# Optimization experiments

Measured on AMD Instinct MI355X. Metric: run time of the kernel, lower is better.

Reference implementation:

```python
import jax, jax.numpy as jnp
import numpy as np

N_SAMPLES = 32768
CHANNELS = 128
N_ATOMS = 512
ATOM_SIZE = 512
N_TRANSFERS = 64
TRANSFER_SIZE = 8192
N_EVENTS = 32
N_ROOMS = 8
DILATIONS = (1, 3, 9, 27, 1)
BATCH = 8


def _conv1d(x, w, padding, dil=1):
    # x: [B,C,T], w: [O,I,K]
    return jax.lax.conv_general_dilated(
        x, w, (1,), padding, rhs_dilation=(dil,),
        dimension_numbers=('NCH', 'OIH', 'NCH'))


def _fft_convolve(a, b):
    # linear convolution along last dim, truncated to original length
    n = a.shape[-1]
    af = jnp.fft.rfft(a, n=2 * n)
    bf = jnp.fft.rfft(b, n=2 * n)
    return jnp.fft.irfft(af * bf, n=2 * n)[..., :n]


def _mlp(x, hw, hb, ow, ob):
    # LinearOutputStack: 3 hidden Linear(C,C)+leaky_relu, then Linear(C,out)
    for i in range(hw.shape[0]):
        x = jax.nn.leaky_relu(x @ hw[i] + hb[i], 0.2)
    return x @ ow + ob


def setup_inputs() -> dict:
    key = jax.random.key(0)
    ks = jax.random.split(key, 25)
    s = 0.02
    C = CHANNELS
    return {
        'x': jax.random.normal(ks[0], (BATCH, 1, N_SAMPLES), jnp.float32),
        'bank': jax.random.normal(ks[1], (C, 1, 512), jnp.float32) * s,
        'w_net': jax.random.normal(ks[2], (len(DILATIONS), C, C, 3), jnp.float32) * s,
        'b_net': jnp.zeros((len(DILATIONS), C), jnp.float32),
        'attn_w': jax.random.normal(ks[3], (1, C, 1), jnp.float32) * s,
        'attn_b': jnp.zeros((1,), jnp.float32),
        'atoms_hw': jax.random.normal(ks[4], (3, C, C), jnp.float32) * s,
        'atoms_hb': jnp.zeros((3, C), jnp.float32),
        'atoms_ow': jax.random.normal(ks[5], (C, N_ATOMS), jnp.float32) * s,
        'atoms_ob': jnp.zeros((N_ATOMS,), jnp.float32),
        'trans_hw': jax.random.normal(ks[6], (3, C, C), jnp.float32) * s,
        'trans_hb': jnp.zeros((3, C), jnp.float32),
        'trans_ow': jax.random.normal(ks[7], (C, N_TRANSFERS), jnp.float32) * s,
        'trans_ob': jnp.zeros((N_TRANSFERS,), jnp.float32),
        'amp_hw': jax.random.normal(ks[8], (3, C, C), jnp.float32) * s,
        'amp_hb': jnp.zeros((3, C), jnp.float32),
        'amp_ow': jax.random.normal(ks[9], (C, 1), jnp.float32) * s,
        'amp_ob': jnp.zeros((1,), jnp.float32),
        'atoms_dict': jax.random.uniform(ks[10], (N_ATOMS, ATOM_SIZE), jnp.float32, -1.0, 1.0),
        'transfer_dict': jax.random.normal(ks[11], (N_TRANSFERS, TRANSFER_SIZE), jnp.float32) * 0.01,
        'rooms': jax.random.normal(ks[12], (N_ROOMS, N_SAMPLES), jnp.float32) * 0.01,
        'room_w': jax.random.normal(ks[13], (C, N_ROOMS), jnp.float32) * s,
        'room_b': jnp.zeros((N_ROOMS,), jnp.float32),
        'mix_w': jax.random.normal(ks[14], (C, 1), jnp.float32) * s,
        'mix_b': jnp.zeros((1,), jnp.float32),
    }


def reference(x, bank, w_net, b_net, attn_w, attn_b,
              atoms_hw, atoms_hb, atoms_ow, atoms_ob,
              trans_hw, trans_hb, trans_ow, trans_ob,
              amp_hw, amp_hb, amp_ow, amp_ob,
              atoms_dict, transfer_dict, rooms, room_w, room_b, mix_w, mix_b):
    B = x.shape[0]
    # front-end filter bank, padding=256, truncate to n_samples
    h = _conv1d(x, bank, [(256, 256)])[..., :N_SAMPLES]            # [B,C,T]
    # DilatedStack: residual dilated convs
    for i, d in enumerate(DILATIONS):
        h = h + jax.nn.leaky_relu(
            _conv1d(h, w_net[i], 'SAME', d) + b_net[i][None, :, None], 0.2)
    # ExampleNorm: per-example std normalization
    h = h / (jnp.std(h, axis=(1, 2), keepdims=True) + 1e-8)
    context = jnp.max(h, axis=-1)                                   # [B,C]
    attn = jax.nn.sigmoid(_conv1d(h, attn_w, 'SAME') + attn_b[None, :, None])[:, 0, :]  # [B,T]
    # sparsify_vectors: top-k attention positions, latents scaled by attn
    vals, idx = jax.lax.top_k(attn, N_EVENTS)                        # [B,E]
    lat = jnp.take_along_axis(jnp.swapaxes(h, 1, 2), idx[..., None], axis=1) * vals[..., None]  # [B,E,C]
    atoms = jax.nn.softmax(_mlp(lat, atoms_hw, atoms_hb, atoms_ow, atoms_ob), axis=-1) @ atoms_dict
    transfers = jax.nn.softmax(_mlp(lat, trans_hw, trans_hb, trans_ow, trans_ob), axis=-1) @ transfer_dict
    amps = _mlp(lat, amp_hw, amp_hb, amp_ow, amp_ob) ** 2            # [B,E,1]
    atoms = jnp.pad(atoms, ((0, 0), (0, 0), (0, TRANSFER_SIZE - ATOM_SIZE)))
    ev = (_fft_convolve(atoms, transfers) + atoms) * amps            # [B,E,Ts]
    # overlap-add scatter. NOTE: faithful to the original, which does
    # output[:, :, idx:idx+Ts] += x[i, e] -- every event accumulates into a
    # buffer shared across the whole batch.
    pos = idx.reshape(-1)[:, None] + jnp.arange(TRANSFER_SIZE)[None, :]  # [B*E,Ts]
    buf = jnp.zeros(2 * N_SAMPLES, ev.dtype).at[pos].add(ev.reshape(-1, TRANSFER_SIZE))
    dry = jnp.broadcast_to(buf[:N_SAMPLES][None, :], (B, N_SAMPLES))  # [B,T]
    # ReverbGenerator: context -> room choice + wet/dry mix
    impulse = jax.nn.softmax(context @ room_w + room_b, axis=-1) @ rooms  # [B,T]
    mix = jax.nn.sigmoid(context @ mix_w + mix_b)                     # [B,1]
    wet = _fft_convolve(dry, impulse)
    out = dry * (1.0 - mix) + wet * mix
    return out[:, None, :]
```

## Files before the change

### kernel.cpp

```cpp
#include <hip/hip_runtime.h>
#include <math.h>

#define TSAMP 32768
#define CCH 128
#define NBATCH 8
#define NEV 32
#define NROWS 256
#define NATOMS 512
#define ASIZE 512
#define NTRANS 64
#define TSIZE 8192

#define DRY_SCALE 16777216.0f
#define IMP_SCALE 64.0f
#define WET_DESCALE 9.313225746154785e-10f

typedef _Float16 f16x8 __attribute__((ext_vector_type(8)));
typedef _Float16 f16x4 __attribute__((ext_vector_type(4)));
typedef float f32x4 __attribute__((ext_vector_type(4)));


__global__ void k_zs(double* __restrict__ sums) {
  if (threadIdx.x < 16) sums[threadIdx.x] = 0.0;
}

__global__ __launch_bounds__(256) void k_zero(float* __restrict__ wet,
                                              float* __restrict__ dry) {
  int i = blockIdx.x * 256 + threadIdx.x;
  if (i < NBATCH * TSAMP) wet[i] = 0.f;
  if (i < TSAMP) dry[i] = 0.f;
}

__global__ __launch_bounds__(256) void k_wsplit(const float* __restrict__ wn,
                                                _Float16* __restrict__ whi,
                                                _Float16* __restrict__ wlo) {
  const int i = blockIdx.x * 256 + threadIdx.x;
  if (i >= 245760) return;
  const int ci = i & 127;
  int r = i >> 7;
  const int o = r & 127;
  r >>= 7;
  const int k = r % 3;
  const int l = r / 3;
  const float w = wn[(((size_t)l*128 + o)*128 + ci)*3 + k];
  const _Float16 hi = (_Float16)w;
  whi[i] = hi;
  wlo[i] = (_Float16)(w - (float)hi);
}

__global__ __launch_bounds__(256) void k_bsplit(const float* __restrict__ bank,
                                                _Float16* __restrict__ bhi,
                                                _Float16* __restrict__ blo) {
  const int i = blockIdx.x * 256 + threadIdx.x;
  if (i < 65536) {
    const float w = bank[i];
    const _Float16 hi = (_Float16)w;
    bhi[i] = hi;
    blo[i] = (_Float16)(w - (float)hi);
  }
}

__global__ __launch_bounds__(256) void k_front_mfma(
    const float* __restrict__ x, const _Float16* __restrict__ bhi,
    const _Float16* __restrict__ blo, float* __restrict__ h) {
  __shared__ _Float16 shi[8*664];
  __shared__ _Float16 slo[8*664];
  const int t0 = blockIdx.x * 128;
  const int b  = blockIdx.y;
  const float* xb = x + (size_t)b*TSAMP;
  const int tid = threadIdx.x;

  for (int flat = tid; flat < 8*632; flat += 256) {
    const int p = flat / 632;
    const int q = flat - p*632;
    const int g = t0 - 256 + q + p;
    const float v = (g >= 0 && g < TSAMP) ? xb[g] : 0.f;
    const _Float16 hi = (_Float16)v;
    shi[p*664 + q] = hi;
    slo[p*664 + q] = (_Float16)(v - (float)hi);
  }
  __syncthreads();

  const int wv = tid >> 6;
  const int lane = tid & 63;
  const int n = lane & 15;
  const int quad = lane >> 4;
  const int c0 = wv * 32;
  const int ph = n & 7;
  const int nb = n & 8;

  f32x4 acc[2][8];
#pragma unroll
  for (int i = 0; i < 2; ++i)
#pragma unroll
    for (int j = 0; j < 8; ++j) acc[i][j] = (f32x4){0.f,0.f,0.f,0.f};

  for (int kc = 0; kc < 16; ++kc) {
    const int kb = kc*32 + quad*8;
    f16x8 ahi[2], alo[2];
#pragma unroll
    for (int os = 0; os < 2; ++os) {
      const size_t ao = (size_t)(c0 + os*16 + n)*512 + kb;
      ahi[os] = *(const f16x8*)(bhi + ao);
      alo[os] = *(const f16x8*)(blo + ao);
    }
#pragma unroll
    for (int tg = 0; tg < 2; ++tg) {
      f16x8 xh[4], xl[4];
#pragma unroll
      for (int u = 0; u < 4; ++u) {
        const int a = ph*664 + (tg*4 + u)*16 + nb + kb;
        xh[u] = *(const f16x8*)(shi + a);
        xl[u] = *(const f16x8*)(slo + a);
      }
#pragma unroll
      for (int os = 0; os < 2; ++os)
#pragma unroll
        for (int u = 0; u < 4; ++u) {
          f32x4 a4 = acc[os][tg*4 + u];
          a4 = __builtin_amdgcn_mfma_f32_16x16x32_f16(ahi[os], xh[u], a4, 0, 0, 0);
          a4 = __builtin_amdgcn_mfma_f32_16x16x32_f16(alo[os], xh[u], a4, 0, 0, 0);
          a4 = __builtin_amdgcn_mfma_f32_16x16x32_f16(ahi[os], xl[u], a4, 0, 0, 0);
          acc[os][tg*4 + u] = a4;
        }
    }
  }

  float* hb = h + (size_t)b*TSAMP*CCH;
#pragma unroll
  for (int os = 0; os < 2; ++os) {
    const int cb = c0 + os*16 + quad*4;
#pragma unroll
    for (int ts = 0; ts < 8; ++ts) {
      const int t = t0 + ts*16 + n;
      *(f32x4*)(hb + (size_t)t*CCH + cb) = acc[os][ts];
    }
  }
}

__global__ __launch_bounds__(256) void k_dil_mfma(
    const float* __restrict__ hin0, const _Float16* __restrict__ whi,
    const _Float16* __restrict__ wlo, const float* __restrict__ bias,
    float* __restrict__ hout0, const int d) {
  extern __shared__ _Float16 sh[];
  const int twin = 64 + 2*d;
  _Float16* shi = sh;
  _Float16* slo = sh + twin*136;
  const int t0 = blockIdx.x * 64;
  const size_t bs = (size_t)blockIdx.y * CCH * TSAMP;
  const float* __restrict__ hin = hin0 + bs;
  float* __restrict__ hout = hout0 + bs;
  const int tid = threadIdx.x;

  for (int flat = tid; flat < twin*32; flat += 256) {
    const int tw = flat >> 5;
    const int c4 = (flat & 31) << 2;
    const int g = t0 - d + tw;
    float4 v = {0.f, 0.f, 0.f, 0.f};
    if (g >= 0 && g < TSAMP) v = *(const float4*)(hin + (size_t)g*CCH + c4);
    f16x4 hv, lv;
    hv[0] = (_Float16)v.x; hv[1] = (_Float16)v.y;
    hv[2] = (_Float16)v.z; hv[3] = (_Float16)v.w;
    lv[0] = (_Float16)(v.x - (float)hv[0]); lv[1] = (_Float16)(v.y - (float)hv[1]);
    lv[2] = (_Float16)(v.z - (float)hv[2]); lv[3] = (_Float16)(v.w - (float)hv[3]);
    *(f16x4*)(shi + tw*136 + c4) = hv;
    *(f16x4*)(slo + tw*136 + c4) = lv;
  }
  __syncthreads();

  const int wv = tid >> 6;
  const int lane = tid & 63;
  const int n = lane & 15;
  const int quad = lane >> 4;
  const int o0 = wv * 32;

  f32x4 acc[2][4];
#pragma unroll
  for (int i = 0; i < 2; ++i)
#pragma unroll
    for (int j = 0; j < 4; ++j) acc[i][j] = (f32x4){0.f,0.f,0.f,0.f};

  for (int k = 0; k < 3; ++k) {
    for (int kc = 0; kc < 4; ++kc) {
      const int cib = kc*32 + quad*8;
      f16x8 ahi[2], alo[2];
#pragma unroll
      for (int os = 0; os < 2; ++os) {
        const size_t wo = ((size_t)k*128 + (o0 + os*16 + n))*128 + cib;
        ahi[os] = *(const f16x8*)(whi + wo);
        alo[os] = *(const f16x8*)(wlo + wo);
      }
      f16x8 bhi[4], blo[4];
#pragma unroll
      for (int ts = 0; ts < 4; ++ts) {
        const int a = (ts*16 + n + k*d)*136 + cib;
        bhi[ts] = *(const f16x8*)(shi + a);
        blo[ts] = *(const f16x8*)(slo + a);
      }
#pragma unroll
      for (int os = 0; os < 2; ++os)
#pragma unroll
        for (int ts = 0; ts < 4; ++ts) {
          acc[os][ts] = __builtin_amdgcn_mfma_f32_16x16x32_f16(ahi[os], bhi[ts], acc[os][ts], 0, 0, 0);
          acc[os][ts] = __builtin_amdgcn_mfma_f32_16x16x32_f16(alo[os], bhi[ts], acc[os][ts], 0, 0, 0);
          acc[os][ts] = __builtin_amdgcn_mfma_f32_16x16x32_f16(ahi[os], blo[ts], acc[os][ts], 0, 0, 0);
        }
    }
  }

#pragma unroll
  for (int os = 0; os < 2; ++os) {
    const int ob = o0 + os*16 + quad*4;
    const f32x4 bs4 = *(const f32x4*)(bias + ob);
#pragma unroll
    for (int ts = 0; ts < 4; ++ts) {
      const int t = t0 + ts*16 + n;
      const int tw = ts*16 + n + d;
      const f16x4 phv = *(const f16x4*)(shi + tw*136 + ob);
      const f16x4 plv = *(const f16x4*)(slo + tw*136 + ob);
      f32x4 res;
#pragma unroll
      for (int r = 0; r < 4; ++r) {
        float v = acc[os][ts][r] + bs4[r];
        v = v > 0.f ? v : 0.2f*v;
        res[r] = (float)phv[r] + (float)plv[r] + v;
      }
      *(f32x4*)(hout + (size_t)t*CCH + ob) = res;
    }
  }
}

__global__ __launch_bounds__(256) void k_dil_last(
    const float* __restrict__ hin0, const _Float16* __restrict__ whi,
    const _Float16* __restrict__ wlo, const float* __restrict__ bias,
    float* __restrict__ hout0, const int d,
    const float* __restrict__ aw, double* __restrict__ sums,
    float* __restrict__ attnraw, float* __restrict__ pm, const int bb0) {
  extern __shared__ _Float16 sh[];
  const int twin = 64 + 2*d;
  _Float16* shi = sh;
  _Float16* slo = sh + twin*136;
  __shared__ float attl[4*64];
  __shared__ double sred[8];
  const int t0 = blockIdx.x * 64;
  const int b = bb0 + blockIdx.y;
  const size_t bs = (size_t)blockIdx.y * CCH * TSAMP;
  const float* __restrict__ hin = hin0 + bs;
  float* __restrict__ hout = hout0 + bs;
  const int tid = threadIdx.x;

  for (int flat = tid; flat < twin*32; flat += 256) {
    const int tw = flat >> 5;
    const int c4 = (flat & 31) << 2;
    const int g = t0 - d + tw;
    float4 v = {0.f, 0.f, 0.f, 0.f};
    if (g >= 0 && g < TSAMP) v = *(const float4*)(hin + (size_t)g*CCH + c4);
    f16x4 hv, lv;
    hv[0] = (_Float16)v.x; hv[1] = (_Float16)v.y;
    hv[2] = (_Float16)v.z; hv[3] = (_Float16)v.w;
    lv[0] = (_Float16)(v.x - (float)hv[0]); lv[1] = (_Float16)(v.y - (float)hv[1]);
    lv[2] = (_Float16)(v.z - (float)hv[2]); lv[3] = (_Float16)(v.w - (float)hv[3]);
    *(f16x4*)(shi + tw*136 + c4) = hv;
    *(f16x4*)(slo + tw*136 + c4) = lv;
  }
  __syncthreads();

  const int wv = tid >> 6;
  const int lane = tid & 63;
  const int n = lane & 15;
  const int quad = lane >> 4;
  const int o0 = wv * 32;

  f32x4 acc[2][4];
#pragma unroll
  for (int i = 0; i < 2; ++i)
#pragma unroll
    for (int j = 0; j < 4; ++j) acc[i][j] = (f32x4){0.f,0.f,0.f,0.f};

  for (int k = 0; k < 3; ++k) {
    for (int kc = 0; kc < 4; ++kc) {
      const int cib = kc*32 + quad*8;
      f16x8 ahi[2], alo[2];
#pragma unroll
      for (int os = 0; os < 2; ++os) {
        const size_t wo = ((size_t)k*128 + (o0 + os*16 + n))*128 + cib;
        ahi[os] = *(const f16x8*)(whi + wo);
        alo[os] = *(const f16x8*)(wlo + wo);
      }
      f16x8 bhi[4], blo[4];
#pragma unroll
      for (int ts = 0; ts < 4; ++ts) {
        const int a = (ts*16 + n + k*d)*136 + cib;
        bhi[ts] = *(const f16x8*)(shi + a);
        blo[ts] = *(const f16x8*)(slo + a);
      }
#pragma unroll
      for (int os = 0; os < 2; ++os)
#pragma unroll
        for (int ts = 0; ts < 4; ++ts) {
          acc[os][ts] = __builtin_amdgcn_mfma_f32_16x16x32_f16(ahi[os], bhi[ts], acc[os][ts], 0, 0, 0);
          acc[os][ts] = __builtin_amdgcn_mfma_f32_16x16x32_f16(alo[os], bhi[ts], acc[os][ts], 0, 0, 0);
          acc[os][ts] = __builtin_amdgcn_mfma_f32_16x16x32_f16(ahi[os], blo[ts], acc[os][ts], 0, 0, 0);
        }
    }
  }

  const f32x4 awq0 = *(const f32x4*)(aw + o0 + quad*4);
  const f32x4 awq1 = *(const f32x4*)(aw + o0 + 16 + quad*4);
  double s = 0.0, s2 = 0.0;
  float pa[4] = {0.f, 0.f, 0.f, 0.f};
  f32x4 cm[2];
  cm[0] = (f32x4){-3.4e38f, -3.4e38f, -3.4e38f, -3.4e38f};
  cm[1] = cm[0];

#pragma unroll
  for (int os = 0; os < 2; ++os) {
    const int ob = o0 + os*16 + quad*4;
    const f32x4 bs4 = *(const f32x4*)(bias + ob);
    const f32x4 awv = os ? awq1 : awq0;
#pragma unroll
    for (int ts = 0; ts < 4; ++ts) {
      const int t = t0 + ts*16 + n;
      const int tw = ts*16 + n + d;
      const f16x4 phv = *(const f16x4*)(shi + tw*136 + ob);
      const f16x4 plv = *(const f16x4*)(slo + tw*136 + ob);
      f32x4 res;
      float dotp = 0.f;
#pragma unroll
      for (int r = 0; r < 4; ++r) {
        float v = acc[os][ts][r] + bs4[r];
        v = v > 0.f ? v : 0.2f*v;
        const float hv = (float)phv[r] + (float)plv[r] + v;
        res[r] = hv;
        s += (double)hv; s2 += (double)hv*(double)hv;
        dotp += hv * awv[r];
        cm[os][r] = fmaxf(cm[os][r], hv);
      }
      pa[ts] += dotp;
      *(f32x4*)(hout + (size_t)t*CCH + ob) = res;
    }
  }

#pragma unroll
  for (int ts = 0; ts < 4; ++ts) {
    pa[ts] += __shfl_xor(pa[ts], 16);
    pa[ts] += __shfl_xor(pa[ts], 32);
  }
  if (quad == 0) {
#pragma unroll
    for (int ts = 0; ts < 4; ++ts) attl[wv*64 + ts*16 + n] = pa[ts];
  }
#pragma unroll
  for (int mk = 1; mk <= 8; mk <<= 1)
#pragma unroll
    for (int os = 0; os < 2; ++os)
#pragma unroll
      for (int r = 0; r < 4; ++r)
        cm[os][r] = fmaxf(cm[os][r], __shfl_xor(cm[os][r], mk));
  if (n == 0) {
#pragma unroll
    for (int os = 0; os < 2; ++os)
      *(f32x4*)(pm + ((size_t)b*512 + blockIdx.x)*128 + o0 + os*16 + quad*4) = cm[os];
  }
  for (int sft = 32; sft; sft >>= 1) { s += __shfl_down(s, sft); s2 += __shfl_down(s2, sft); }
  if (lane == 0) { sred[wv*2] = s; sred[wv*2+1] = s2; }
  __syncthreads();
  if (tid < 64)
    attnraw[(size_t)b*TSAMP + t0 + tid] =
        attl[tid] + attl[64 + tid] + attl[128 + tid] + attl[192 + tid];
  if (tid == 0) {
    atomicAdd(&sums[b*2],   sred[0] + sred[2] + sred[4] + sred[6]);
    atomicAdd(&sums[b*2+1], sred[1] + sred[3] + sred[5] + sred[7]);
  }
}

__global__ void k_scale(const double* __restrict__ sums, float* __restrict__ scal) {
  const int b = threadIdx.x;
  if (b < NBATCH) {
    const double n = (double)CCH * (double)TSAMP;
    const double mean = sums[b*2] / n;
    double var = sums[b*2+1] / n - mean*mean;
    if (var < 0.0) var = 0.0;
    scal[b] = (float)(1.0 / (sqrt(var) + 1e-8));
  }
}

__global__ void k_context2(const float* __restrict__ pm, const float* __restrict__ scal,
                           float* __restrict__ ctx) {
  const int b = blockIdx.x;
  const int c = threadIdx.x;
  float m = -3.4e38f;
  for (int s = 0; s < 512; ++s) m = fmaxf(m, pm[((size_t)b*512 + s)*128 + c]);
  ctx[b*128 + c] = m * scal[b];
}

__global__ __launch_bounds__(256) void k_attn2(const float* __restrict__ raw,
                                               const float* __restrict__ scal,
                                               const float* __restrict__ ab,
                                               float* __restrict__ attn) {
  const int b = blockIdx.y;
  const int i = blockIdx.x*1024 + threadIdx.x*4;
  const float s = scal[b], bb = ab[0];
  const float4 v = *(const float4*)(raw + (size_t)b*TSAMP + i);
  float* o = attn + (size_t)b*TSAMP + i;
  o[0] = 1.f/(1.f+expf(-(v.x*s+bb)));
  o[1] = 1.f/(1.f+expf(-(v.y*s+bb)));
  o[2] = 1.f/(1.f+expf(-(v.z*s+bb)));
  o[3] = 1.f/(1.f+expf(-(v.w*s+bb)));
}

__global__ __launch_bounds__(256) void k_topk1(const float* __restrict__ attn,
                                               float* __restrict__ cv,
                                               int* __restrict__ cidx) {
  const int ch = blockIdx.x, b = blockIdx.y;
  const float* a = attn + (size_t)b*TSAMP + ch*4096;
  __shared__ float v[4096];
  __shared__ float rv[4]; __shared__ int ri[4];
  const int tid = threadIdx.x;
  for (int i = tid; i < 4096; i += 256) v[i] = a[i];
  __syncthreads();
  for (int e = 0; e < NEV; ++e) {
    float bv = -1e30f; int bi = 0;
    for (int i = tid; i < 4096; i += 256) {
      const float x = v[i];
      if (x > bv) { bv = x; bi = i; }
    }
    for (int s = 32; s; s >>= 1) {
      const float ov = __shfl_down(bv, s); const int oi = __shfl_down(bi, s);
      if (ov > bv || (ov == bv && oi < bi)) { bv = ov; bi = oi; }
    }
    if ((tid & 63) == 0) { rv[tid >> 6] = bv; ri[tid >> 6] = bi; }
    __syncthreads();
    if (tid == 0) {
      int bb = 0;
      for (int w2 = 1; w2 < 4; ++w2)
        if (rv[w2] > rv[bb] || (rv[w2] == rv[bb] && ri[w2] < ri[bb])) bb = w2;
      cv[(b*8 + ch)*NEV + e] = rv[bb];
      cidx[(b*8 + ch)*NEV + e] = ch*4096 + ri[bb];
      v[ri[bb]] = -1e30f;
    }
    __syncthreads();
  }
}

__global__ __launch_bounds__(256) void k_topk2(const float* __restrict__ cv,
                                               const int* __restrict__ ci_,
                                               float* __restrict__ vals,
                                               int* __restrict__ idxs) {
  const int b = blockIdx.x;
  const int tid = threadIdx.x;
  float my = cv[b*256 + tid];
  int   mi = ci_[b*256 + tid];
  __shared__ float rv[4]; __shared__ int ri[4];
  __shared__ float bvs; __shared__ int bis;
  for (int e = 0; e < NEV; ++e) {
    float bv = my; int bi = mi;
    for (int s = 32; s; s >>= 1) {
      const float ov = __shfl_down(bv, s); const int oi = __shfl_down(bi, s);
      if (ov > bv || (ov == bv && oi < bi)) { bv = ov; bi = oi; }
    }
    if ((tid & 63) == 0) { rv[tid >> 6] = bv; ri[tid >> 6] = bi; }
    __syncthreads();
    if (tid == 0) {
      int bb = 0;
      for (int w2 = 1; w2 < 4; ++w2)
        if (rv[w2] > rv[bb] || (rv[w2] == rv[bb] && ri[w2] < ri[bb])) bb = w2;
      vals[b*NEV + e] = rv[bb]; idxs[b*NEV + e] = ri[bb];
      bvs = rv[bb]; bis = ri[bb];
    }
    __syncthreads();
    if (mi == bis && my == bvs) my = -1e30f;
    __syncthreads();
  }
}

__device__ __forceinline__ float blk_max128(float v, float* red) {
  const int tid = threadIdx.x;
  red[tid] = v; __syncthreads();
  for (int s = 64; s > 0; s >>= 1) {
    if (tid < s) red[tid] = fmaxf(red[tid], red[tid + s]);
    __syncthreads();
  }
  const float r = red[0]; __syncthreads();
  return r;
}
__device__ __forceinline__ float blk_sum128(float v, float* red) {
  const int tid = threadIdx.x;
  red[tid] = v; __syncthreads();
  for (int s = 64; s > 0; s >>= 1) {
    if (tid < s) red[tid] += red[tid + s];
    __syncthreads();
  }
  const float r = red[0]; __syncthreads();
  return r;
}
__device__ __forceinline__ float mlp_hidden3(float latv, const float* __restrict__ hw,
                                             const float* __restrict__ hb, float* xa) {
  const int tid = threadIdx.x;
  float cur = latv;
  for (int i = 0; i < 3; ++i) {
    xa[tid] = cur; __syncthreads();
    const float* W = hw + (size_t)i*CCH*CCH;
    float acc = hb[i*CCH + tid];
    for (int c = 0; c < CCH; ++c) acc += xa[c] * W[c*CCH + tid];
    cur = acc > 0.f ? acc : 0.2f*acc;
    __syncthreads();
  }
  return cur;
}

__global__ __launch_bounds__(128) void k_mlp(
    const float* __restrict__ h, const float* __restrict__ scal,
    const float* __restrict__ vals, const int* __restrict__ idxs,
    const float* __restrict__ a_hw, const float* __restrict__ a_hb,
    const float* __restrict__ a_ow, const float* __restrict__ a_ob,
    const float* __restrict__ t_hw, const float* __restrict__ t_hb,
    const float* __restrict__ t_ow, const float* __restrict__ t_ob,
    const float* __restrict__ m_hw, const float* __restrict__ m_hb,
    const float* __restrict__ m_ow, const float* __restrict__ m_ob,
    float* __restrict__ p_atoms, float* __restrict__ p_trans, float* __restrict__ amps) {
  const int row = blockIdx.x;
  const int b = row >> 5;
  const int tid = threadIdx.x;
  __shared__ float xa[CCH];
  __shared__ float red[CCH];
  const int t = idxs[row];
  const float latv = h[((size_t)b*TSAMP + t)*CCH + tid] * scal[b] * vals[row];

  {
    const float cur = mlp_hidden3(latv, a_hw, a_hb, xa);
    xa[tid] = cur; __syncthreads();
    float l0 = a_ob[tid], l1 = a_ob[tid+128], l2 = a_ob[tid+256], l3 = a_ob[tid+384];
    for (int c = 0; c < CCH; ++c) {
      const float xv = xa[c];
      const float* W = a_ow + (size_t)c*NATOMS + tid;
      l0 += xv*W[0]; l1 += xv*W[128]; l2 += xv*W[256]; l3 += xv*W[384];
    }
    const float mx = blk_max128(fmaxf(fmaxf(l0,l1), fmaxf(l2,l3)), red);
    const float e0 = expf(l0-mx), e1 = expf(l1-mx), e2 = expf(l2-mx), e3 = expf(l3-mx);
    const float inv = 1.f / blk_sum128(e0+e1+e2+e3, red);
    float* pa = p_atoms + (size_t)row*NATOMS;
    pa[tid] = e0*inv; pa[tid+128] = e1*inv; pa[tid+256] = e2*inv; pa[tid+384] = e3*inv;
  }
  {
    const float cur = mlp_hidden3(latv, t_hw, t_hb, xa);
    xa[tid] = cur; __syncthreads();
    float lg = -3.4e38f;
    if (tid < NTRANS) {
      float acc = t_ob[tid];
      for (int c = 0; c < CCH; ++c) acc += xa[c]*t_ow[c*NTRANS + tid];
      lg = acc;
    }
    const float mt = blk_max128(lg, red);
    const float et = (tid < NTRANS) ? expf(lg - mt) : 0.f;
    const float st = blk_sum128(et, red);
    if (tid < NTRANS) p_trans[(size_t)row*NTRANS + tid] = et/st;
  }
  {
    const float cur = mlp_hidden3(latv, m_hw, m_hb, xa);
    const float s = blk_sum128(cur * m_ow[tid], red);
    if (tid == 0) { const float v = s + m_ob[0]; amps[row] = v*v; }
  }
}

__global__ __launch_bounds__(256) void k_atoms_mm(const float* __restrict__ p_atoms,
                                                  const float* __restrict__ dict,
                                                  float* __restrict__ av) {
  const int row = blockIdx.x;
  __shared__ float p[NATOMS];
  for (int i = threadIdx.x; i < NATOMS; i += 256) p[i] = p_atoms[(size_t)row*NATOMS + i];
  __syncthreads();
  const int s0 = threadIdx.x*2;
  float a0=0, a1=0;
  for (int a = 0; a < NATOMS; ++a) {
    const float pa = p[a];
    const float2 dv = *(const float2*)(dict + (size_t)a*ASIZE + s0);
    a0 += pa*dv.x; a1 += pa*dv.y;
  }
  av[(size_t)row*ASIZE + s0] = a0; av[(size_t)row*ASIZE + s0 + 1] = a1;
}

__global__ __launch_bounds__(256) void k_trans_mm(const float* __restrict__ p_trans,
                                                   const float* __restrict__ td,
                                                   float* __restrict__ trans) {
  const int row = blockIdx.y;
  const int t = blockIdx.x*2048 + threadIdx.x*8;
  __shared__ float p[NTRANS];
  if (threadIdx.x < NTRANS) p[threadIdx.x] = p_trans[(size_t)row*NTRANS + threadIdx.x];
  __syncthreads();
  float a0=0,a1=0,a2=0,a3=0,a4=0,a5=0,a6=0,a7=0;
  for (int j = 0; j < NTRANS; ++j) {
    const float pj = p[j];
    const float4 v0 = *(const float4*)(td + (size_t)j*TSIZE + t);
    const float4 v1 = *(const float4*)(td + (size_t)j*TSIZE + t + 4);
    a0 += pj*v0.x; a1 += pj*v0.y; a2 += pj*v0.z; a3 += pj*v0.w;
    a4 += pj*v1.x; a5 += pj*v1.y; a6 += pj*v1.z; a7 += pj*v1.w;
  }
  float* o = trans + (size_t)row*TSIZE + t;
  o[0]=a0; o[1]=a1; o[2]=a2; o[3]=a3; o[4]=a4; o[5]=a5; o[6]=a6; o[7]=a7;
}

__global__ __launch_bounds__(256) void k_ev(const float* __restrict__ trans,
                                            const float* __restrict__ av,
                                            const float* __restrict__ amps,
                                            float* __restrict__ ev) {
  const int row = blockIdx.y;
  const int t0 = blockIdx.x * 1024;
  __shared__ float al[512];
  __shared__ float tw[1536];
  for (int i = threadIdx.x; i < 512; i += 256) al[i] = av[(size_t)row*ASIZE + i];
  for (int i = threadIdx.x; i < 1536; i += 256) {
    const int g = t0 - 512 + i;
    tw[i] = (g >= 0) ? trans[(size_t)row*TSIZE + g] : 0.f;
  }
  __syncthreads();
  const int base = threadIdx.x*4 + 512;
  float a0=0,a1=0,a2=0,a3=0;
  float w0=tw[base], w1=tw[base+1], w2=tw[base+2], w3=tw[base+3];
#pragma unroll 8
  for (int k = 0; k < 512; ++k) {
    const float ak = al[k];
    a0 += ak*w0; a1 += ak*w1; a2 += ak*w2; a3 += ak*w3;
    w3 = w2; w2 = w1; w1 = w0; w0 = tw[base - k - 1];
  }
  const int n = t0 + threadIdx.x*4;
  const float amp = amps[row];
  float* e = ev + (size_t)row*TSIZE + n;
  e[0] = (a0 + (n+0 < 512 ? al[n+0] : 0.f)) * amp;
  e[1] = (a1 + (n+1 < 512 ? al[n+1] : 0.f)) * amp;
  e[2] = (a2 + (n+2 < 512 ? al[n+2] : 0.f)) * amp;
  e[3] = (a3 + (n+3 < 512 ? al[n+3] : 0.f)) * amp;
}

__global__ __launch_bounds__(256) void k_dry(const float* __restrict__ ev,
                                             const int* __restrict__ idxs,
                                             float* __restrict__ dry) {
  __shared__ int sidx[32];
  const int r0 = blockIdx.y * 32;
  if (threadIdx.x < 32) sidx[threadIdx.x] = idxs[r0 + threadIdx.x];
  __syncthreads();
  const int p = blockIdx.x*512 + threadIdx.x*2;
  float a0=0,a1=0;
  for (int r = 0; r < 32; ++r) {
    const int off = p - sidx[r];
    if (off >= -1 && off < TSIZE) {
      const float* er = ev + (size_t)(r0 + r)*TSIZE;
      if ((unsigned)(off  ) < TSIZE) a0 += er[off];
      if ((unsigned)(off+1) < TSIZE) a1 += er[off+1];
    }
  }
  atomicAdd(dry + p,     a0);
  atomicAdd(dry + p + 1, a1);
}

__global__ __launch_bounds__(256) void k_dryrev(const float* __restrict__ dry,
                                                _Float16* __restrict__ drev) {
  const int i = blockIdx.x*256 + threadIdx.x;
  if (i < TSAMP + 1088)
    drev[i] = (i < TSAMP) ? (_Float16)(dry[TSAMP-1-i] * DRY_SCALE) : (_Float16)0.f;
}

__global__ void k_room(const float* __restrict__ ctx, const float* __restrict__ room_w,
                       const float* __restrict__ room_b, const float* __restrict__ mix_w,
                       const float* __restrict__ mix_b, float* __restrict__ roomp,
                       float* __restrict__ mix) {
  const int b = threadIdx.x >> 3;
  const int r = threadIdx.x & 7;
  float acc = room_b[r];
  for (int c = 0; c < CCH; ++c) acc += ctx[b*CCH + c] * room_w[c*8 + r];
  float m = acc;
  for (int s = 1; s < 8; s <<= 1) m = fmaxf(m, __shfl_xor(m, s, 8));
  const float e = expf(acc - m);
  float ssum = e;
  for (int s = 1; s < 8; s <<= 1) ssum += __shfl_xor(ssum, s, 8);
  roomp[b*8 + r] = e / ssum;
  if (r == 0) {
    float a = mix_b[0];
    for (int c = 0; c < CCH; ++c) a += ctx[b*CCH + c] * mix_w[c];
    mix[b] = 1.f/(1.f+expf(-a));
  }
}

__global__ __launch_bounds__(256) void k_impulse(const float* __restrict__ roomp,
                                                 const float* __restrict__ rooms,
                                                 _Float16* __restrict__ ihi) {
  const int b = blockIdx.y;
  const int t = blockIdx.x*1024 + threadIdx.x*4;
  float a0=0,a1=0,a2=0,a3=0;
  for (int r = 0; r < 8; ++r) {
    const float pr = roomp[b*8 + r];
    const float4 v = *(const float4*)(rooms + (size_t)r*TSAMP + t);
    a0 += pr*v.x; a1 += pr*v.y; a2 += pr*v.z; a3 += pr*v.w;
  }
  _Float16* oh = ihi + (size_t)b*TSAMP + t;
  oh[0] = (_Float16)(a0*IMP_SCALE); oh[1] = (_Float16)(a1*IMP_SCALE);
  oh[2] = (_Float16)(a2*IMP_SCALE); oh[3] = (_Float16)(a3*IMP_SCALE);
}

__global__ __launch_bounds__(256) void k_wet_mfma(
    const _Float16* __restrict__ drev, const _Float16* __restrict__ ihi,
    float* __restrict__ wet) {
  const int t0 = blockIdx.x * 512;
  const int k0 = blockIdx.y * 4096;
  if (k0 > t0 + 511) return;
  __shared__ _Float16 rhi[8*1048];
  const int tid = threadIdx.x;
  const int wv = tid >> 6;
  const int lane = tid & 63;
  const int n16 = lane & 15;
  const int quad = lane >> 4;
  const int m = n16;

  f32x4 acc[8];
#pragma unroll
  for (int j = 0; j < 8; ++j) acc[j] = (f32x4){0.f,0.f,0.f,0.f};

  const int kend = (k0 + 4096 < t0 + 512) ? k0 + 4096 : t0 + 512;
  const int ph = 7 - (n16 & 7);
  for (int kc0 = k0; kc0 < kend; kc0 += 512) {
    const int RB = TSAMP - 1 - (t0 + 511 - kc0);
    for (int flat = tid; flat < 8*1016; flat += 256) {
      const int p = flat / 1016;
      const int q = flat - p*1016;
      rhi[p*1048 + q] = drev[RB + p + q];
    }
    __syncthreads();

#pragma unroll 4
    for (int kc = 0; kc < 16; ++kc) {
      const int kb = kc*32;
      const int jg = kc0 + kb + quad*8;
      f16x8 ah;
      if (m < NBATCH) ah = *(const f16x8*)(ihi + (size_t)m*TSAMP + jg);
      else ah = (f16x8){0,0,0,0,0,0,0,0};
#pragma unroll
      for (int ts = 0; ts < 8; ++ts) {
        const int nn = wv*128 + ts*16 + n16;
        const int a = ph*1048 + kb + quad*8 + 504 - (nn & ~7);
        const f16x8 bh = *(const f16x8*)(rhi + a);
        acc[ts] = __builtin_amdgcn_mfma_f32_16x16x32_f16(ah, bh, acc[ts], 0, 0, 0);
      }
    }
    __syncthreads();
  }

#pragma unroll
  for (int ts = 0; ts < 8; ++ts) {
    const int t = t0 + wv*128 + ts*16 + n16;
#pragma unroll
    for (int r = 0; r < 4; ++r) {
      const int b = quad*4 + r;
      if (b < NBATCH)
        atomicAdd(wet + (size_t)b*TSAMP + t, acc[ts][r] * WET_DESCALE);
    }
  }
}

__global__ __launch_bounds__(256) void k_out(const float* __restrict__ dry,
                                             const float* __restrict__ wet,
                                             const float* __restrict__ mix,
                                             float* __restrict__ out) {
  const int b = blockIdx.y;
  const int t = blockIdx.x*1024 + threadIdx.x*4;
  const float m = mix[b];
  const float4 d = *(const float4*)(dry + t);
  const float4 w = *(const float4*)(wet + (size_t)b*TSAMP + t);
  float* o = out + (size_t)b*TSAMP + t;
  o[0] = d.x*(1.f-m) + w.x*m;
  o[1] = d.y*(1.f-m) + w.y*m;
  o[2] = d.z*(1.f-m) + w.z*m;
  o[3] = d.w*(1.f-m) + w.w*m;
}

extern "C" void kernel_launch(void* const* d_in, const int* in_sizes, int n_in,
                              void* d_out, int out_size, void* d_ws, size_t ws_size,
                              hipStream_t stream) {
  (void)in_sizes; (void)n_in; (void)out_size; (void)ws_size;
  const float* x      = (const float*)d_in[0];
  const float* bank   = (const float*)d_in[1];
  const float* w_net  = (const float*)d_in[2];
  const float* b_net  = (const float*)d_in[3];
  const float* attn_w = (const float*)d_in[4];
  const float* attn_b = (const float*)d_in[5];
  const float* a_hw = (const float*)d_in[6];
  const float* a_hb = (const float*)d_in[7];
  const float* a_ow = (const float*)d_in[8];
  const float* a_ob = (const float*)d_in[9];
  const float* t_hw = (const float*)d_in[10];
  const float* t_hb = (const float*)d_in[11];
  const float* t_ow = (const float*)d_in[12];
  const float* t_ob = (const float*)d_in[13];
  const float* m_hw = (const float*)d_in[14];
  const float* m_hb = (const float*)d_in[15];
  const float* m_ow = (const float*)d_in[16];
  const float* m_ob = (const float*)d_in[17];
  const float* atoms_dict    = (const float*)d_in[18];
  const float* transfer_dict = (const float*)d_in[19];
  const float* rooms  = (const float*)d_in[20];
  const float* room_w = (const float*)d_in[21];
  const float* room_b = (const float*)d_in[22];
  const float* mix_w  = (const float*)d_in[23];
  const float* mix_b  = (const float*)d_in[24];
  float* out = (float*)d_out;

  float* ws = (float*)d_ws;
  float* H  = ws;
  float* t1 = ws + (size_t)33554432;
  float* t2 = ws + (size_t)41943040;
  _Float16* whi = (_Float16*)(ws + (size_t)50331648);
  _Float16* wlo = (_Float16*)(ws + (size_t)50454528);
  _Float16* bhi = (_Float16*)(ws + (size_t)50577408);
  _Float16* blo = (_Float16*)(ws + (size_t)50610176);
  double* sums  = (double*)(ws + (size_t)50642944);
  float* attnraw = ws + (size_t)50642976;
  float* pm      = ws + (size_t)50905120;

  size_t off = 33554432;
  float* attn  = ws + off; off += (size_t)NBATCH*TSAMP;
  float* scal  = ws + off; off += 8;
  float* ctx   = ws + off; off += NBATCH*CCH;
  float* vals  = ws + off; off += NROWS;
  int*   idxs  = (int*)(ws + off); off += NROWS;
  float* p_atoms = ws + off; off += (size_t)NROWS*NATOMS;
  float* p_trans = ws + off; off += (size_t)NROWS*NTRANS;
  float* amps  = ws + off; off += NROWS;
  float* av    = ws + off; off += (size_t)NROWS*ASIZE;
  float* trans = ws + off; off += (size_t)NROWS*TSIZE;
  float* ev    = ws + off; off += (size_t)NROWS*TSIZE;
  float* dry   = ws + off; off += TSAMP;
  float* roomp = ws + off; off += 64;
  float* mix   = ws + off; off += 8;
  float* wet   = ws + off; off += (size_t)NBATCH*TSAMP;
  float* cand_v = ws + off; off += 2048;
  int*   cand_i = (int*)(ws + off); off += 2048;
  _Float16* imphi = (_Float16*)(ws + off); off += (size_t)NBATCH*TSAMP/2;
  _Float16* drev  = (_Float16*)(ws + off); off += (TSAMP + 1088)/2 + 4;

  k_zs<<<1, 64, 0, stream>>>(sums);
  k_wsplit<<<960, 256, 0, stream>>>(w_net, whi, wlo);
  k_bsplit<<<256, 256, 0, stream>>>(bank, bhi, blo);
  k_front_mfma<<<dim3(256, 8), 256, 0, stream>>>(x, bhi, blo, H);

  const int dil[5] = {1, 3, 9, 27, 1};
  const size_t S = (size_t)CCH * TSAMP;
  for (int p = 0; p < 4; ++p) {
    float* Hp = H + (size_t)(2*p) * S;
    float* io[6] = {Hp, t1, t2, t1, t2, Hp};
    for (int i = 0; i < 4; ++i) {
      const int d = dil[i];
      const size_t smem = (size_t)(64 + 2*d) * 544;
      k_dil_mfma<<<dim3(512, 2), 256, smem, stream>>>(
          io[i], whi + (size_t)i*49152, wlo + (size_t)i*49152, b_net + i*CCH,
          io[i+1], d);
    }
    {
      const int d = dil[4];
      const size_t smem = (size_t)(64 + 2*d) * 544;
      k_dil_last<<<dim3(512, 2), 256, smem, stream>>>(
          io[4], whi + (size_t)4*49152, wlo + (size_t)4*49152, b_net + 4*CCH,
          io[5], d, attn_w, sums, attnraw, pm, 2*p);
    }
  }

  k_zero<<<1024, 256, 0, stream>>>(wet, dry);
  k_scale<<<1, 64, 0, stream>>>(sums, scal);
  k_context2<<<8, 128, 0, stream>>>(pm, scal, ctx);
  k_attn2<<<dim3(32, 8), 256, 0, stream>>>(attnraw, scal, attn_b, attn);
  k_topk1<<<dim3(8, 8), 256, 0, stream>>>(attn, cand_v, cand_i);
  k_topk2<<<8, 256, 0, stream>>>(cand_v, cand_i, vals, idxs);
  k_mlp<<<256, 128, 0, stream>>>(H, scal, vals, idxs,
                                 a_hw, a_hb, a_ow, a_ob,
                                 t_hw, t_hb, t_ow, t_ob,
                                 m_hw, m_hb, m_ow, m_ob,
                                 p_atoms, p_trans, amps);
  k_atoms_mm<<<256, 256, 0, stream>>>(p_atoms, atoms_dict, av);
  k_trans_mm<<<dim3(4, 256), 256, 0, stream>>>(p_trans, transfer_dict, trans);
  k_ev<<<dim3(8, 256), 256, 0, stream>>>(trans, av, amps, ev);
  k_dry<<<dim3(64, 8), 256, 0, stream>>>(ev, idxs, dry);
  k_dryrev<<<133, 256, 0, stream>>>(dry, drev);
  k_room<<<1, 64, 0, stream>>>(ctx, room_w, room_b, mix_w, mix_b, roomp, mix);
  k_impulse<<<dim3(32, 8), 256, 0, stream>>>(roomp, rooms, imphi);
  k_wet_mfma<<<dim3(64, 8), 256, 0, stream>>>(drev, imphi, wet);
  k_out<<<dim3(32, 8), 256, 0, stream>>>(dry, wet, mix, out);
}
```

Measured before the change: 1.472 ms.

## Widen dilated conv tiles to 128 timesteps, fuse sigmoid into top-k, pad LDS

Adds a k_dil128 kernel, and changes k_dil_last, so each block covers 128 timesteps instead of 64. This reuses each weight fragment across twice as many MFMA tiles and halves the block count. The d=27 layer stays on the old 64-wide kernel, probably to limit shared memory. Separately, the sigmoid attention pass is fused into the first top-k stage, which now uses 16 chunks per batch and feeds a 512-thread second stage. The k_ev transfer window gets padded LDS indexing to avoid bank conflicts. Costs are higher register pressure (16 accumulators per wave) and more shared memory per block, which may lower occupancy.

```diff
diff --git a/kernel.cpp b/kernel.cpp
--- a/kernel.cpp
+++ b/kernel.cpp
@@ -14,6 +14,8 @@
 #define DRY_SCALE 16777216.0f
 #define IMP_SCALE 64.0f
 #define WET_DESCALE 9.313225746154785e-10f
+
+#define EPAD(i) ((i) + ((i) >> 5))
 
 typedef _Float16 f16x8 __attribute__((ext_vector_type(8)));
 typedef _Float16 f16x4 __attribute__((ext_vector_type(4)));
@@ -230,20 +232,15 @@
   }
 }
 
-__global__ __launch_bounds__(256) void k_dil_last(
+__global__ __launch_bounds__(256) void k_dil128(
     const float* __restrict__ hin0, const _Float16* __restrict__ whi,
     const _Float16* __restrict__ wlo, const float* __restrict__ bias,
-    float* __restrict__ hout0, const int d,
-    const float* __restrict__ aw, double* __restrict__ sums,
-    float* __restrict__ attnraw, float* __restrict__ pm, const int bb0) {
+    float* __restrict__ hout0, const int d) {
   extern __shared__ _Float16 sh[];
-  const int twin = 64 + 2*d;
+  const int twin = 128 + 2*d;
   _Float16* shi = sh;
   _Float16* slo = sh + twin*136;
-  __shared__ float attl[4*64];
-  __shared__ double sred[8];
-  const int t0 = blockIdx.x * 64;
-  const int b = bb0 + blockIdx.y;
+  const int t0 = blockIdx.x * 128;
   const size_t bs = (size_t)blockIdx.y * CCH * TSAMP;
   const float* __restrict__ hin = hin0 + bs;
   float* __restrict__ hout = hout0 + bs;
@@ -271,11 +268,11 @@
   const int quad = lane >> 4;
   const int o0 = wv * 32;
 
-  f32x4 acc[2][4];
+  f32x4 acc[2][8];
 #pragma unroll
   for (int i = 0; i < 2; ++i)
 #pragma unroll
-    for (int j = 0; j < 4; ++j) acc[i][j] = (f32x4){0.f,0.f,0.f,0.f};
+    for (int j = 0; j < 8; ++j) acc[i][j] = (f32x4){0.f,0.f,0.f,0.f};
 
   for (int k = 0; k < 3; ++k) {
     for (int kc = 0; kc < 4; ++kc) {
@@ -287,28 +284,135 @@
         ahi[os] = *(const f16x8*)(whi + wo);
         alo[os] = *(const f16x8*)(wlo + wo);
       }
-      f16x8 bhi[4], blo[4];
-#pragma unroll
-      for (int ts = 0; ts < 4; ++ts) {
-        const int a = (ts*16 + n + k*d)*136 + cib;
-        bhi[ts] = *(const f16x8*)(shi + a);
-        blo[ts] = *(const f16x8*)(slo + a);
-      }
-#pragma unroll
-      for (int os = 0; os < 2; ++os)
-#pragma unroll
-        for (int ts = 0; ts < 4; ++ts) {
-          acc[os][ts] = __builtin_amdgcn_mfma_f32_16x16x32_f16(ahi[os], bhi[ts], acc[os][ts], 0, 0, 0);
-          acc[os][ts] = __builtin_amdgcn_mfma_f32_16x16x32_f16(alo[os], bhi[ts], acc[os][ts], 0, 0, 0);
-          acc[os][ts] = __builtin_amdgcn_mfma_f32_16x16x32_f16(ahi[os], blo[ts], acc[os][ts], 0, 0, 0);
+#pragma unroll
+      for (int tg = 0; tg < 2; ++tg) {
+        f16x8 bh[4], bl[4];
+#pragma unroll
+        for (int u = 0; u < 4; ++u) {
+          const int a = ((tg*4 + u)*16 + n + k*d)*136 + cib;
+          bh[u] = *(const f16x8*)(shi + a);
+          bl[u] = *(const f16x8*)(slo + a);
         }
+#pragma unroll
+        for (int os = 0; os < 2; ++os)
+#pragma unroll
+          for (int u = 0; u < 4; ++u) {
+            f32x4 a4 = acc[os][tg*4 + u];
+            a4 = __builtin_amdgcn_mfma_f32_16x16x32_f16(ahi[os], bh[u], a4, 0, 0, 0);
+            a4 = __builtin_amdgcn_mfma_f32_16x16x32_f16(alo[os], bh[u], a4, 0, 0, 0);
+            a4 = __builtin_amdgcn_mfma_f32_16x16x32_f16(ahi[os], bl[u], a4, 0, 0, 0);
+            acc[os][tg*4 + u] = a4;
+          }
+      }
+    }
+  }
+
+#pragma unroll
+  for (int os = 0; os < 2; ++os) {
+    const int ob = o0 + os*16 + quad*4;
+    const f32x4 bs4 = *(const f32x4*)(bias + ob);
+#pragma unroll
+    for (int ts = 0; ts < 8; ++ts) {
+      const int t = t0 + ts*16 + n;
+      const int tw = ts*16 + n + d;
+      const f16x4 phv = *(const f16x4*)(shi + tw*136 + ob);
+      const f16x4 plv = *(const f16x4*)(slo + tw*136 + ob);
+      f32x4 res;
+#pragma unroll
+      for (int r = 0; r < 4; ++r) {
+        float v = acc[os][ts][r] + bs4[r];
+        v = v > 0.f ? v : 0.2f*v;
+        res[r] = (float)phv[r] + (float)plv[r] + v;
+      }
+      *(f32x4*)(hout + (size_t)t*CCH + ob) = res;
+    }
+  }
+}
+
+__global__ __launch_bounds__(256) void k_dil_last(
+    const float* __restrict__ hin0, const _Float16* __restrict__ whi,
+    const _Float16* __restrict__ wlo, const float* __restrict__ bias,
+    float* __restrict__ hout0, const int d,
+    const float* __restrict__ aw, double* __restrict__ sums,
+    float* __restrict__ attnraw, float* __restrict__ pm, const int bb0) {
+  extern __shared__ _Float16 sh[];
+  const int twin = 128 + 2*d;
+  _Float16* shi = sh;
+  _Float16* slo = sh + twin*136;
+  __shared__ float attl[4*128];
+  __shared__ double sred[8];
+  const int t0 = blockIdx.x * 128;
+  const int b = bb0 + blockIdx.y;
+  const size_t bs = (size_t)blockIdx.y * CCH * TSAMP;
+  const float* __restrict__ hin = hin0 + bs;
+  float* __restrict__ hout = hout0 + bs;
+  const int tid = threadIdx.x;
+
+  for (int flat = tid; flat < twin*32; flat += 256) {
+    const int tw = flat >> 5;
+    const int c4 = (flat & 31) << 2;
+    const int g = t0 - d + tw;
+    float4 v = {0.f, 0.f, 0.f, 0.f};
+    if (g >= 0 && g < TSAMP) v = *(const float4*)(hin + (size_t)g*CCH + c4);
+    f16x4 hv, lv;
+    hv[0] = (_Float16)v.x; hv[1] = (_Float16)v.y;
+    hv[2] = (_Float16)v.z; hv[3] = (_Float16)v.w;
+    lv[0] = (_Float16)(v.x - (float)hv[0]); lv[1] = (_Float16)(v.y - (float)hv[1]);
+    lv[2] = (_Float16)(v.z - (float)hv[2]); lv[3] = (_Float16)(v.w - (float)hv[3]);
+    *(f16x4*)(shi + tw*136 + c4) = hv;
+    *(f16x4*)(slo + tw*136 + c4) = lv;
+  }
+  __syncthreads();
+
+  const int wv = tid >> 6;
+  const int lane = tid & 63;
+  const int n = lane & 15;
+  const int quad = lane >> 4;
+  const int o0 = wv * 32;
+
+  f32x4 acc[2][8];
+#pragma unroll
+  for (int i = 0; i < 2; ++i)
+#pragma unroll
+    for (int j = 0; j < 8; ++j) acc[i][j] = (f32x4){0.f,0.f,0.f,0.f};
+
+  for (int k = 0; k < 3; ++k) {
+    for (int kc = 0; kc < 4; ++kc) {
+      const int cib = kc*32 + quad*8;
+      f16x8 ahi[2], alo[2];
+#pragma unroll
+      for (int os = 0; os < 2; ++os) {
+        const size_t wo = ((size_t)k*128 + (o0 + os*16 + n))*128 + cib;
+        ahi[os] = *(const f16x8*)(whi + wo);
+        alo[os] = *(const f16x8*)(wlo + wo);
+      }
+#pragma unroll
+      for (int tg = 0; tg < 2; ++tg) {
+        f16x8 bh[4], bl[4];
+#pragma unroll
+        for (int u = 0; u < 4; ++u) {
+          const int a = ((tg*4 + u)*16 + n + k*d)*136 + cib;
+          bh[u] = *(const f16x8*)(shi + a);
+          bl[u] = *(const f16x8*)(slo + a);
+        }
+#pragma unroll
+        for (int os = 0; os < 2; ++os)
+#pragma unroll
+          for (int u = 0; u < 4; ++u) {
+            f32x4 a4 = acc[os][tg*4 + u];
+            a4 = __builtin_amdgcn_mfma_f32_16x16x32_f16(ahi[os], bh[u], a4, 0, 0, 0);
+            a4 = __builtin_amdgcn_mfma_f32_16x16x32_f16(alo[os], bh[u], a4, 0, 0, 0);
+            a4 = __builtin_amdgcn_mfma_f32_16x16x32_f16(ahi[os], bl[u], a4, 0, 0, 0);
+            acc[os][tg*4 + u] = a4;
+          }
+      }
     }
   }
 
   const f32x4 awq0 = *(const f32x4*)(aw + o0 + quad*4);
   const f32x4 awq1 = *(const f32x4*)(aw + o0 + 16 + quad*4);
   double s = 0.0, s2 = 0.0;
-  float pa[4] = {0.f, 0.f, 0.f, 0.f};
+  float pa[8] = {0.f,0.f,0.f,0.f,0.f,0.f,0.f,0.f};
   f32x4 cm[2];
   cm[0] = (f32x4){-3.4e38f, -3.4e38f, -3.4e38f, -3.4e38f};
   cm[1] = cm[0];
@@ -319,7 +423,7 @@
     const f32x4 bs4 = *(const f32x4*)(bias + ob);
     const f32x4 awv = os ? awq1 : awq0;
 #pragma unroll
-    for (int ts = 0; ts < 4; ++ts) {
+    for (int ts = 0; ts < 8; ++ts) {
       const int t = t0 + ts*16 + n;
       const int tw = ts*16 + n + d;
       const f16x4 phv = *(const f16x4*)(shi + tw*136 + ob);
@@ -342,13 +446,13 @@
   }
 
 #pragma unroll
-  for (int ts = 0; ts < 4; ++ts) {
+  for (int ts = 0; ts < 8; ++ts) {
     pa[ts] += __shfl_xor(pa[ts], 16);
     pa[ts] += __shfl_xor(pa[ts], 32);
   }
   if (quad == 0) {
 #pragma unroll
-    for (int ts = 0; ts < 4; ++ts) attl[wv*64 + ts*16 + n] = pa[ts];
+    for (int ts = 0; ts < 8; ++ts) attl[wv*128 + ts*16 + n] = pa[ts];
   }
 #pragma unroll
   for (int mk = 1; mk <= 8; mk <<= 1)
@@ -360,14 +464,14 @@
   if (n == 0) {
 #pragma unroll
     for (int os = 0; os < 2; ++os)
-      *(f32x4*)(pm + ((size_t)b*512 + blockIdx.x)*128 + o0 + os*16 + quad*4) = cm[os];
+      *(f32x4*)(pm + ((size_t)b*256 + blockIdx.x)*128 + o0 + os*16 + quad*4) = cm[os];
   }
   for (int sft = 32; sft; sft >>= 1) { s += __shfl_down(s, sft); s2 += __shfl_down(s2, sft); }
   if (lane == 0) { sred[wv*2] = s; sred[wv*2+1] = s2; }
   __syncthreads();
-  if (tid < 64)
+  if (tid < 128)
     attnraw[(size_t)b*TSAMP + t0 + tid] =
-        attl[tid] + attl[64 + tid] + attl[128 + tid] + attl[192 + tid];
+        attl[tid] + attl[128 + tid] + attl[256 + tid] + attl[384 + tid];
   if (tid == 0) {
     atomicAdd(&sums[b*2],   sred[0] + sred[2] + sred[4] + sred[6]);
     atomicAdd(&sums[b*2+1], sred[1] + sred[3] + sred[5] + sred[7]);
@@ -390,38 +494,27 @@
   const int b = blockIdx.x;
   const int c = threadIdx.x;
   float m = -3.4e38f;
-  for (int s = 0; s < 512; ++s) m = fmaxf(m, pm[((size_t)b*512 + s)*128 + c]);
+  for (int s = 0; s < 256; ++s) m = fmaxf(m, pm[((size_t)b*256 + s)*128 + c]);
   ctx[b*128 + c] = m * scal[b];
 }
 
-__global__ __launch_bounds__(256) void k_attn2(const float* __restrict__ raw,
+__global__ __launch_bounds__(256) void k_topk1(const float* __restrict__ raw,
                                                const float* __restrict__ scal,
                                                const float* __restrict__ ab,
-                                               float* __restrict__ attn) {
-  const int b = blockIdx.y;
-  const int i = blockIdx.x*1024 + threadIdx.x*4;
-  const float s = scal[b], bb = ab[0];
-  const float4 v = *(const float4*)(raw + (size_t)b*TSAMP + i);
-  float* o = attn + (size_t)b*TSAMP + i;
-  o[0] = 1.f/(1.f+expf(-(v.x*s+bb)));
-  o[1] = 1.f/(1.f+expf(-(v.y*s+bb)));
-  o[2] = 1.f/(1.f+expf(-(v.z*s+bb)));
-  o[3] = 1.f/(1.f+expf(-(v.w*s+bb)));
-}
-
-__global__ __launch_bounds__(256) void k_topk1(const float* __restrict__ attn,
                                                float* __restrict__ cv,
                                                int* __restrict__ cidx) {
   const int ch = blockIdx.x, b = blockIdx.y;
-  const float* a = attn + (size_t)b*TSAMP + ch*4096;
-  __shared__ float v[4096];
+  const float sc = scal[b], bb_ = ab[0];
+  const float* a = raw + (size_t)b*TSAMP + ch*2048;
+  __shared__ float v[2048];
   __shared__ float rv[4]; __shared__ int ri[4];
   const int tid = threadIdx.x;
-  for (int i = tid; i < 4096; i += 256) v[i] = a[i];
+  for (int i = tid; i < 2048; i += 256)
+    v[i] = 1.f/(1.f+expf(-(a[i]*sc + bb_)));
   __syncthreads();
   for (int e = 0; e < NEV; ++e) {
     float bv = -1e30f; int bi = 0;
-    for (int i = tid; i < 4096; i += 256) {
+    for (int i = tid; i < 2048; i += 256) {
       const float x = v[i];
       if (x > bv) { bv = x; bi = i; }
     }
@@ -435,23 +528,23 @@
       int bb = 0;
       for (int w2 = 1; w2 < 4; ++w2)
         if (rv[w2] > rv[bb] || (rv[w2] == rv[bb] && ri[w2] < ri[bb])) bb = w2;
-      cv[(b*8 + ch)*NEV + e] = rv[bb];
-      cidx[(b*8 + ch)*NEV + e] = ch*4096 + ri[bb];
+      cv[(b*16 + ch)*NEV + e] = rv[bb];
+      cidx[(b*16 + ch)*NEV + e] = ch*2048 + ri[bb];
       v[ri[bb]] = -1e30f;
     }
     __syncthreads();
   }
 }
 
-__global__ __launch_bounds__(256) void k_topk2(const float* __restrict__ cv,
+__global__ __launch_bounds__(512) void k_topk2(const float* __restrict__ cv,
                                                const int* __restrict__ ci_,
                                                float* __restrict__ vals,
                                                int* __restrict__ idxs) {
   const int b = blockIdx.x;
   const int tid = threadIdx.x;
-  float my = cv[b*256 + tid];
-  int   mi = ci_[b*256 + tid];
-  __shared__ float rv[4]; __shared__ int ri[4];
+  float my = cv[b*512 + tid];
+  int   mi = ci_[b*512 + tid];
+  __shared__ float rv[8]; __shared__ int ri[8];
   __shared__ float bvs; __shared__ int bis;
   for (int e = 0; e < NEV; ++e) {
     float bv = my; int bi = mi;
@@ -463,7 +556,7 @@
     __syncthreads();
     if (tid == 0) {
       int bb = 0;
-      for (int w2 = 1; w2 < 4; ++w2)
+      for (int w2 = 1; w2 < 8; ++w2)
         if (rv[w2] > rv[bb] || (rv[w2] == rv[bb] && ri[w2] < ri[bb])) bb = w2;
       vals[b*NEV + e] = rv[bb]; idxs[b*NEV + e] = ri[bb];
       bvs = rv[bb]; bis = ri[bb];
@@ -607,21 +700,23 @@
   const int row = blockIdx.y;
   const int t0 = blockIdx.x * 1024;
   __shared__ float al[512];
-  __shared__ float tw[1536];
+  __shared__ float tw[1584];
   for (int i = threadIdx.x; i < 512; i += 256) al[i] = av[(size_t)row*ASIZE + i];
   for (int i = threadIdx.x; i < 1536; i += 256) {
     const int g = t0 - 512 + i;
-    tw[i] = (g >= 0) ? trans[(size_t)row*TSIZE + g] : 0.f;
+    tw[EPAD(i)] = (g >= 0) ? trans[(size_t)row*TSIZE + g] : 0.f;
   }
   __syncthreads();
   const int base = threadIdx.x*4 + 512;
   float a0=0,a1=0,a2=0,a3=0;
-  float w0=tw[base], w1=tw[base+1], w2=tw[base+2], w3=tw[base+3];
+  float w0=tw[EPAD(base)], w1=tw[EPAD(base+1)], w2=tw[EPAD(base+2)], w3=tw[EPAD(base+3)];
 #pragma unroll 8
   for (int k = 0; k < 512; ++k) {
     const float ak = al[k];
     a0 += ak*w0; a1 += ak*w1; a2 += ak*w2; a3 += ak*w3;
-    w3 = w2; w2 = w1; w1 = w0; w0 = tw[base - k - 1];
+    w3 = w2; w2 = w1; w1 = w0;
+    const int p = base - k - 1;
+    w0 = tw[EPAD(p)];
   }
   const int n = t0 + threadIdx.x*4;
   const float amp = amps[row];
@@ -816,7 +911,6 @@
   float* pm      = ws + (size_t)50905120;
 
   size_t off = 33554432;
-  float* attn  = ws + off; off += (size_t)NBATCH*TSAMP;
   float* scal  = ws + off; off += 8;
   float* ctx   = ws + off; off += NBATCH*CCH;
   float* vals  = ws + off; off += NROWS;
@@ -831,8 +925,8 @@
   float* roomp = ws + off; off += 64;
   float* mix   = ws + off; off += 8;
   float* wet   = ws + off; off += (size_t)NBATCH*TSAMP;
-  float* cand_v = ws + off; off += 2048;
-  int*   cand_i = (int*)(ws + off); off += 2048;
+  float* cand_v = ws + off; off += 4096;
+  int*   cand_i = (int*)(ws + off); off += 4096;
   _Float16* imphi = (_Float16*)(ws + off); off += (size_t)NBATCH*TSAMP/2;
   _Float16* drev  = (_Float16*)(ws + off); off += (TSAMP + 1088)/2 + 4;
 
@@ -846,17 +940,24 @@
   for (int p = 0; p < 4; ++p) {
     float* Hp = H + (size_t)(2*p) * S;
     float* io[6] = {Hp, t1, t2, t1, t2, Hp};
-    for (int i = 0; i < 4; ++i) {
+    for (int i = 0; i < 3; ++i) {
       const int d = dil[i];
+      const size_t smem = (size_t)(128 + 2*d) * 544;
+      k_dil128<<<dim3(256, 2), 256, smem, stream>>>(
+          io[i], whi + (size_t)i*49152, wlo + (size_t)i*49152, b_net + i*CCH,
+          io[i+1], d);
+    }
+    {
+      const int d = dil[3];
       const size_t smem = (size_t)(64 + 2*d) * 544;
       k_dil_mfma<<<dim3(512, 2), 256, smem, stream>>>(
-          io[i], whi + (size_t)i*49152, wlo + (size_t)i*49152, b_net + i*CCH,
-          io[i+1], d);
+          io[3], whi + (size_t)3*49152, wlo + (size_t)3*49152, b_net + 3*CCH,
+          io[4], d);
     }
     {
       const int d = dil[4];
-      const size_t smem = (size_t)(64 + 2*d) * 544;
-      k_dil_last<<<dim3(512, 2), 256, smem, stream>>>(
+      const size_t smem = (size_t)(128 + 2*d) * 544;
+      k_dil_last<<<dim3(256, 2), 256, smem, stream>>>(
           io[4], whi + (size_t)4*49152, wlo + (size_t)4*49152, b_net + 4*CCH,
           io[5], d, attn_w, sums, attnraw, pm, 2*p);
     }
@@ -865,9 +966,8 @@
   k_zero<<<1024, 256, 0, stream>>>(wet, dry);
   k_scale<<<1, 64, 0, stream>>>(sums, scal);
   k_context2<<<8, 128, 0, stream>>>(pm, scal, ctx);
-  k_attn2<<<dim3(32, 8), 256, 0, stream>>>(attnraw, scal, attn_b, attn);
-  k_topk1<<<dim3(8, 8), 256, 0, stream>>>(attn, cand_v, cand_i);
-  k_topk2<<<8, 256, 0, stream>>>(cand_v, cand_i, vals, idxs);
+  k_topk1<<<dim3(16, 8), 256, 0, stream>>>(attnraw, scal, attn_b, cand_v, cand_i);
+  k_topk2<<<8, 512, 0, stream>>>(cand_v, cand_i, vals, idxs);
   k_mlp<<<256, 128, 0, stream>>>(H, scal, vals, idxs,
                                  a_hw, a_hb, a_ow, a_ob,
                                  t_hw, t_hb, t_ow, t_ob,
```

Result: faster. 1.210 ms (-17.8%).
